# Optimization experiments

Hardware: AMD Instinct MI355X
Metric: run time of the kernel (lower is better)

Reference implementation:

```python
import jax, jax.numpy as jnp
import numpy as np

B = 1024           # number of jets (independent binary trees)
L = 10             # tree depth (levels); level j has B*2**j nodes
H = 128            # hidden size
FEAT = 7           # input features per node
LEVEL_SIZES = [B * 2**j for j in range(L)]
OFF = np.concatenate([[0], np.cumsum(LEVEL_SIZES)]).astype(int).tolist()
INNER = LEVEL_SIZES[:-1]                     # all non-bottom nodes are inner
COFF = np.concatenate([[0], np.cumsum(INNER)]).astype(int).tolist()


def _linear_init(key, fan_in, fan_out):
    return jax.random.normal(key, (fan_in, fan_out), jnp.float32) / np.sqrt(fan_in).astype(np.float32)


def setup_inputs() -> dict:
    key = jax.random.key(0)
    ks = jax.random.split(key, 6)
    contents = jax.random.normal(ks[0], (OFF[-1], FEAT), jnp.float32)
    # child indices are local to level j+1: node k at level j -> children (2k, 2k+1)
    ch = [np.stack([2 * np.arange(n), 2 * np.arange(n) + 1], axis=1) for n in INNER]
    children = jnp.asarray(np.concatenate(ch, axis=0), jnp.int32)
    return {
        "contents": contents,
        "children": children,
        "W_u": _linear_init(ks[1], FEAT, H), "b_u": jnp.zeros((H,), jnp.float32),
        "W_h": _linear_init(ks[2], 3 * H, H), "b_h": jnp.zeros((H,), jnp.float32),
        "W_z": _linear_init(ks[3], 4 * H, 4 * H), "b_z": jnp.zeros((4 * H,), jnp.float32),
        "W_r": _linear_init(ks[4], 3 * H, 3 * H), "b_r": jnp.zeros((3 * H,), jnp.float32),
        "conv_w": jnp.asarray([0.9], jnp.float32),
        "conv_b": jnp.asarray([0.01], jnp.float32),
    }


def reference(contents, children, W_u, b_u, W_h, b_h, W_z, b_z, W_r, b_r, conv_w, conv_b):
    def conv_chain(x):
        # relu(conv1x1(relu(conv1x1(relu(conv1x1(x)))))): Conv2d(1,1,1) == scalar scale + bias
        for _ in range(3):
            x = jax.nn.relu(conv_w[0] * x + conv_b[0])
        return x

    emb = None  # embeddings of the level below (level j+1)
    for j in reversed(range(L)):
        c = contents[OFF[j]:OFF[j + 1]]               # [N_j, FEAT]
        u = conv_chain(c @ W_u + b_u)                 # [N_j, H]
        if j == L - 1:                                # bottom level: all leaves
            emb = u
            continue
        ch = children[COFF[j]:COFF[j + 1]]            # [N_j, 2] indices into level j+1
        h_L = emb[ch[:, 0]]                           # gather left children
        h_R = emb[ch[:, 1]]                           # gather right children
        hhu = jnp.concatenate([h_L, h_R, u], axis=1)  # [N_j, 3H]
        r = jax.nn.sigmoid(hhu @ W_r + b_r)           # reset gate
        h_H = conv_chain((r * hhu) @ W_h + b_h)       # [N_j, H]
        z = jnp.concatenate([h_H, hhu], axis=1) @ W_z + b_z  # [N_j, 4H]
        g = jax.nn.softmax(
            jnp.stack([z[:, :H], z[:, H:2 * H], z[:, 2 * H:3 * H], z[:, 3 * H:]], axis=-1),
            axis=-1,
        )                                             # [N_j, H, 4] gate weights
        emb = g[..., 0] * h_H + g[..., 1] * h_L + g[..., 2] * h_R + g[..., 3] * u
    return emb.reshape(B, -1)                         # [B, H] root embeddings
```

## Files before the change

### kernel.cpp

```cpp
#include <hip/hip_runtime.h>
#include <hip/hip_bf16.h>

typedef _Float16 f16x8 __attribute__((ext_vector_type(8)));
typedef _Float16 f16x4 __attribute__((ext_vector_type(4)));
typedef float f32x4 __attribute__((ext_vector_type(4)));

#define H 128
#define FEAT 7
#define RB 64
#define NT 512

__device__ __forceinline__ float conv3(float x, float w, float b) {
    x = fmaxf(fmaf(w, x, b), 0.f);
    x = fmaxf(fmaf(w, x, b), 0.f);
    x = fmaxf(fmaf(w, x, b), 0.f);
    return x;
}
__device__ __forceinline__ float sigm(float x) {
    return __builtin_amdgcn_rcpf(1.f + __expf(-x));
}

__global__ __launch_bounds__(256) void pack_weights(
    const float* __restrict__ Wr, const float* __restrict__ Wh, const float* __restrict__ Wz,
    _Float16* __restrict__ Pr, _Float16* __restrict__ Ph, _Float16* __restrict__ Pz)
{
    int idx = blockIdx.x * 256 + threadIdx.x;
    if (idx < 384 * 384) {
        int k = idx / 384, n = idx % 384;
        Pr[((size_t)(k >> 3) * 384 + n) * 8 + (k & 7)] = (_Float16)Wr[idx];
    }
    if (idx < 384 * 128) {
        int k = idx / 128, n = idx % 128;
        Ph[((size_t)(k >> 3) * 128 + n) * 8 + (k & 7)] = (_Float16)Wh[idx];
    }
    if (idx < 512 * 512) {
        int k = idx / 512, n = idx % 512;
        Pz[((size_t)(k >> 3) * 512 + n) * 8 + (k & 7)] = (_Float16)Wz[idx];
    }
}

template<bool LEAF>
__global__ __launch_bounds__(NT, 2) void level_kernel(
    const float* __restrict__ contents,
    const int* __restrict__ children,
    const float* __restrict__ leafContents,
    const _Float16* __restrict__ embPrev,
    _Float16* __restrict__ embOut,
    float* __restrict__ finalOut,
    const float* __restrict__ Wu, const float* __restrict__ bu,
    const _Float16* __restrict__ Pr, const float* __restrict__ br,
    const _Float16* __restrict__ Ph, const float* __restrict__ bh,
    const _Float16* __restrict__ Pz, const float* __restrict__ bz,
    const float* __restrict__ convw, const float* __restrict__ convb)
{
    __shared__ __align__(16) _Float16 s_hhu[RB][392];
    __shared__ __align__(16) _Float16 s_x[RB][392];
    _Float16 (* const s_hH)[136] = (_Float16 (*)[136])&s_x[0][0];

    const int t = threadIdx.x;
    const int row0 = blockIdx.x * RB;
    const int col0 = t & 127;
    const int tq = t >> 7;
    const float cw = convw[0], cbv = convb[0];

    float wcol[FEAT];
#pragma unroll
    for (int k = 0; k < FEAT; k++) wcol[k] = Wu[k * H + col0];
    const float bucol = bu[col0];

#pragma unroll 4
    for (int i = 0; i < 16; i++) {
        int r = i * 4 + tq;
        const float* c = contents + (size_t)(row0 + r) * FEAT;
        float acc = bucol;
#pragma unroll
        for (int k = 0; k < FEAT; k++) acc = fmaf(c[k], wcol[k], acc);
        s_hhu[r][256 + col0] = (_Float16)conv3(acc, cw, cbv);
    }

    if (LEAF) {
#pragma unroll 4
        for (int i = 0; i < 32; i++) {
            int cr = i * 4 + tq;
            int child = children[row0 * 2 + cr];
            const float* c = leafContents + (size_t)child * FEAT;
            float acc = bucol;
#pragma unroll
            for (int k = 0; k < FEAT; k++) acc = fmaf(c[k], wcol[k], acc);
            s_hhu[cr >> 1][(cr & 1) * 128 + col0] = (_Float16)conv3(acc, cw, cbv);
        }
    } else {
        int rp = t >> 4, chunk = t & 15;
#pragma unroll
        for (int p = 0; p < 4; p++) {
            int cr = p * 32 + rp;
            int child = children[row0 * 2 + cr];
            uint4 v = *(const uint4*)(embPrev + (size_t)child * H + chunk * 8);
            *(uint4*)&s_hhu[cr >> 1][(cr & 1) * 128 + chunk * 8] = v;
        }
    }
    __syncthreads();

    const int lane = t & 63;
    const int w = t >> 6;
    const int q = lane >> 4;
    const int ln = lane & 15;

    {
        const f16x8* PB = (const f16x8*)Pr + (w * 48 + ln);
        f32x4 acc[3][4];
#pragma unroll
        for (int c = 0; c < 3; c++)
#pragma unroll
            for (int rt = 0; rt < 4; rt++) acc[c][rt] = (f32x4){0,0,0,0};
        f16x8 b[4];
#pragma unroll
        for (int rt = 0; rt < 4; rt++) b[rt] = *(const f16x8*)&s_hhu[rt * 16 + ln][q * 8];
        f16x8 an[3];
#pragma unroll
        for (int c = 0; c < 3; c++) an[c] = PB[(size_t)q * 384 + c * 16];
#pragma unroll
        for (int kk = 0; kk < 12; kk++) {
            f16x8 cb[4], ac[3];
#pragma unroll
            for (int rt = 0; rt < 4; rt++) cb[rt] = b[rt];
#pragma unroll
            for (int c = 0; c < 3; c++) ac[c] = an[c];
            if (kk < 11) {
                int kb = (kk + 1) * 4 + q;
#pragma unroll
                for (int c = 0; c < 3; c++) an[c] = PB[(size_t)kb * 384 + c * 16];
#pragma unroll
                for (int rt = 0; rt < 4; rt++)
                    b[rt] = *(const f16x8*)&s_hhu[rt * 16 + ln][(kk + 1) * 32 + q * 8];
            }
#pragma unroll
            for (int c = 0; c < 3; c++)
#pragma unroll
                for (int rt = 0; rt < 4; rt++)
                    acc[c][rt] = __builtin_amdgcn_mfma_f32_16x16x32_f16(ac[c], cb[rt], acc[c][rt], 0, 0, 0);
        }
#pragma unroll
        for (int c = 0; c < 3; c++) {
            int fb = w * 48 + c * 16 + q * 4;
            f32x4 bv = *(const f32x4*)&br[fb];
#pragma unroll
            for (int rt = 0; rt < 4; rt++) {
                int row = rt * 16 + ln;
                f16x4 hh = *(const f16x4*)&s_hhu[row][fb];
                f16x4 xv;
#pragma unroll
                for (int reg = 0; reg < 4; reg++) {
                    float rv = sigm(acc[c][rt][reg] + bv[reg]);
                    xv[reg] = (_Float16)(rv * (float)hh[reg]);
                }
                *(f16x4*)&s_x[row][fb] = xv;
            }
        }
    }
    __syncthreads();

    {
        const f16x8* PB = (const f16x8*)Ph + (w * 16 + ln);
        f32x4 acc[4];
#pragma unroll
        for (int rt = 0; rt < 4; rt++) acc[rt] = (f32x4){0,0,0,0};
        f16x8 b[4];
#pragma unroll
        for (int rt = 0; rt < 4; rt++) b[rt] = *(const f16x8*)&s_x[rt * 16 + ln][q * 8];
        f16x8 an = PB[(size_t)q * 128];
#pragma unroll
        for (int kk = 0; kk < 12; kk++) {
            f16x8 cb[4];
#pragma unroll
            for (int rt = 0; rt < 4; rt++) cb[rt] = b[rt];
            f16x8 ac = an;
            if (kk < 11) {
                int kb = (kk + 1) * 4 + q;
                an = PB[(size_t)kb * 128];
#pragma unroll
                for (int rt = 0; rt < 4; rt++)
                    b[rt] = *(const f16x8*)&s_x[rt * 16 + ln][(kk + 1) * 32 + q * 8];
            }
#pragma unroll
            for (int rt = 0; rt < 4; rt++)
                acc[rt] = __builtin_amdgcn_mfma_f32_16x16x32_f16(ac, cb[rt], acc[rt], 0, 0, 0);
        }
        float hv[4][4];
        int fb = w * 16 + q * 4;
        f32x4 bhv = *(const f32x4*)&bh[fb];
#pragma unroll
        for (int rt = 0; rt < 4; rt++)
#pragma unroll
            for (int reg = 0; reg < 4; reg++)
                hv[rt][reg] = conv3(acc[rt][reg] + bhv[reg], cw, cbv);
        __syncthreads();
#pragma unroll
        for (int rt = 0; rt < 4; rt++) {
            f16x4 hp;
#pragma unroll
            for (int reg = 0; reg < 4; reg++) hp[reg] = (_Float16)hv[rt][reg];
            *(f16x4*)&s_hH[rt * 16 + ln][fb] = hp;
        }
    }
    __syncthreads();

    {
        const int nb = w * 16;
        const f16x8* PL = (const f16x8*)Pz + nb + ln;
        f32x4 acc[4][4];
#pragma unroll
        for (int g = 0; g < 4; g++)
#pragma unroll
            for (int rt = 0; rt < 4; rt++) acc[g][rt] = (f32x4){0,0,0,0};
        f16x8 b[4];
#pragma unroll
        for (int rt = 0; rt < 4; rt++) b[rt] = *(const f16x8*)&s_hH[rt * 16 + ln][q * 8];
        f16x8 wn[4];
#pragma unroll
        for (int g = 0; g < 4; g++) wn[g] = PL[(size_t)q * 512 + g * 128];
#pragma unroll
        for (int kk = 0; kk < 16; kk++) {
            f16x8 cb[4], wc[4];
#pragma unroll
            for (int rt = 0; rt < 4; rt++) cb[rt] = b[rt];
#pragma unroll
            for (int g = 0; g < 4; g++) wc[g] = wn[g];
            if (kk < 15) {
                int kb = (kk + 1) * 4 + q;
#pragma unroll
                for (int g = 0; g < 4; g++) wn[g] = PL[(size_t)kb * 512 + g * 128];
                if (kk + 1 < 4) {
#pragma unroll
                    for (int rt = 0; rt < 4; rt++)
                        b[rt] = *(const f16x8*)&s_hH[rt * 16 + ln][(kk + 1) * 32 + q * 8];
                } else {
                    int k0 = (kk + 1) * 32 - 128;
#pragma unroll
                    for (int rt = 0; rt < 4; rt++)
                        b[rt] = *(const f16x8*)&s_hhu[rt * 16 + ln][k0 + q * 8];
                }
            }
#pragma unroll
            for (int g = 0; g < 4; g++)
#pragma unroll
                for (int rt = 0; rt < 4; rt++)
                    acc[g][rt] = __builtin_amdgcn_mfma_f32_16x16x32_f16(wc[g], cb[rt], acc[g][rt], 0, 0, 0);
        }
        int colb = nb + q * 4;
        f32x4 bz0 = *(const f32x4*)&bz[colb];
        f32x4 bz1 = *(const f32x4*)&bz[128 + colb];
        f32x4 bz2 = *(const f32x4*)&bz[256 + colb];
        f32x4 bz3 = *(const f32x4*)&bz[384 + colb];
#pragma unroll
        for (int rt = 0; rt < 4; rt++) {
            int row = rt * 16 + ln;
            f16x4 hH4 = *(const f16x4*)&s_hH[row][colb];
            f16x4 hL4 = *(const f16x4*)&s_hhu[row][colb];
            f16x4 hR4 = *(const f16x4*)&s_hhu[row][128 + colb];
            f16x4 u4  = *(const f16x4*)&s_hhu[row][256 + colb];
            size_t gidx = (size_t)(row0 + row) * H + colb;
            if (finalOut) {
                f32x4 ov;
#pragma unroll
                for (int reg = 0; reg < 4; reg++) {
                    float z0 = acc[0][rt][reg] + bz0[reg];
                    float z1 = acc[1][rt][reg] + bz1[reg];
                    float z2 = acc[2][rt][reg] + bz2[reg];
                    float z3 = acc[3][rt][reg] + bz3[reg];
                    float m = fmaxf(fmaxf(z0, z1), fmaxf(z2, z3));
                    float e0 = __expf(z0 - m), e1 = __expf(z1 - m), e2 = __expf(z2 - m), e3 = __expf(z3 - m);
                    float inv = __builtin_amdgcn_rcpf(e0 + e1 + e2 + e3);
                    ov[reg] = (e0 * (float)hH4[reg] + e1 * (float)hL4[reg] +
                               e2 * (float)hR4[reg] + e3 * (float)u4[reg]) * inv;
                }
                *(f32x4*)&finalOut[gidx] = ov;
            } else {
                f16x4 ev;
#pragma unroll
                for (int reg = 0; reg < 4; reg++) {
                    float z0 = acc[0][rt][reg] + bz0[reg];
                    float z1 = acc[1][rt][reg] + bz1[reg];
                    float z2 = acc[2][rt][reg] + bz2[reg];
                    float z3 = acc[3][rt][reg] + bz3[reg];
                    float m = fmaxf(fmaxf(z0, z1), fmaxf(z2, z3));
                    float e0 = __expf(z0 - m), e1 = __expf(z1 - m), e2 = __expf(z2 - m), e3 = __expf(z3 - m);
                    float inv = __builtin_amdgcn_rcpf(e0 + e1 + e2 + e3);
                    ev[reg] = (_Float16)((e0 * (float)hH4[reg] + e1 * (float)hL4[reg] +
                                          e2 * (float)hR4[reg] + e3 * (float)u4[reg]) * inv);
                }
                *(f16x4*)&embOut[gidx] = ev;
            }
        }
    }
}

extern "C" void kernel_launch(void* const* d_in, const int* in_sizes, int n_in,
                              void* d_out, int out_size, void* d_ws, size_t ws_size,
                              hipStream_t stream) {
    const float* contents = (const float*)d_in[0];
    const int*   children = (const int*)d_in[1];
    const float* Wu = (const float*)d_in[2];
    const float* bu = (const float*)d_in[3];
    const float* Wh = (const float*)d_in[4];
    const float* bh = (const float*)d_in[5];
    const float* Wz = (const float*)d_in[6];
    const float* bz = (const float*)d_in[7];
    const float* Wr = (const float*)d_in[8];
    const float* br = (const float*)d_in[9];
    const float* convw = (const float*)d_in[10];
    const float* convb = (const float*)d_in[11];
    float* out = (float*)d_out;

    _Float16* Pr = (_Float16*)d_ws;
    _Float16* Ph = Pr + 384 * 384;
    _Float16* Pz = Ph + 384 * 128;
    _Float16* bufA = (_Float16*)((char*)d_ws + (1 << 20));
    _Float16* bufB = bufA + (size_t)262144 * H;

    auto OFFS = [](int j) -> long long { return 1024LL * ((1LL << j) - 1); };

    pack_weights<<<(512 * 512 + 255) / 256, 256, 0, stream>>>(Wr, Wh, Wz, Pr, Ph, Pz);

    {
        int n = 1024 << 8;
        level_kernel<true><<<n / RB, NT, 0, stream>>>(
            contents + OFFS(8) * FEAT, children + OFFS(8) * 2,
            contents + OFFS(9) * FEAT, nullptr, bufA, nullptr,
            Wu, bu, Pr, br, Ph, bh, Pz, bz, convw, convb);
    }

    _Float16* prev = bufA;
    _Float16* cur  = bufB;
    for (int j = 7; j >= 0; j--) {
        int n = 1024 << j;
        level_kernel<false><<<n / RB, NT, 0, stream>>>(
            contents + OFFS(j) * FEAT, children + OFFS(j) * 2,
            nullptr, prev, cur, (j == 0 ? out : nullptr),
            Wu, bu, Pr, br, Ph, bh, Pz, bz, convw, convb);
        _Float16* tmp = prev; prev = cur; cur = tmp;
    }
}
```

Baseline: 834.2 us.

## Triple-buffer weight fragment prefetch two k-steps ahead and across GEMM stages

Weight fragments for the three MFMA GEMMs are now loaded two k-steps ahead into a three-slot register ring instead of one step ahead. The first two k-steps of each GEMM's weights are issued during the previous stage, before the embedding load phase and the epilogues, so global-load latency overlaps other work. Row and child indices in the embedding loops are made wave-uniform with readfirstlane so contents loads can become scalar loads. The deeper ring raises register pressure, which could reduce occupancy or cause spills.

```diff
diff --git a/kernel.cpp b/kernel.cpp
--- a/kernel.cpp
+++ b/kernel.cpp
@@ -63,6 +63,18 @@
     const int tq = t >> 7;
     const float cw = convw[0], cbv = convb[0];
 
+    const int lane = t & 63;
+    const int w = t >> 6;
+    const int q = lane >> 4;
+    const int ln = lane & 15;
+
+    const f16x8* PBc = (const f16x8*)Pr + (w * 48 + ln);
+    f16x8 awc[3][3];
+#pragma unroll
+    for (int c = 0; c < 3; c++) awc[0][c] = PBc[(size_t)q * 384 + c * 16];
+#pragma unroll
+    for (int c = 0; c < 3; c++) awc[1][c] = PBc[(size_t)(4 + q) * 384 + c * 16];
+
     float wcol[FEAT];
 #pragma unroll
     for (int k = 0; k < FEAT; k++) wcol[k] = Wu[k * H + col0];
@@ -71,23 +83,25 @@
 #pragma unroll 4
     for (int i = 0; i < 16; i++) {
         int r = i * 4 + tq;
-        const float* c = contents + (size_t)(row0 + r) * FEAT;
+        int ru = __builtin_amdgcn_readfirstlane(r);
+        const float* c = contents + (size_t)(row0 + ru) * FEAT;
         float acc = bucol;
 #pragma unroll
         for (int k = 0; k < FEAT; k++) acc = fmaf(c[k], wcol[k], acc);
-        s_hhu[r][256 + col0] = (_Float16)conv3(acc, cw, cbv);
+        s_hhu[ru][256 + col0] = (_Float16)conv3(acc, cw, cbv);
     }
 
     if (LEAF) {
 #pragma unroll 4
         for (int i = 0; i < 32; i++) {
             int cr = i * 4 + tq;
-            int child = children[row0 * 2 + cr];
+            int cru = __builtin_amdgcn_readfirstlane(cr);
+            int child = __builtin_amdgcn_readfirstlane(children[row0 * 2 + cru]);
             const float* c = leafContents + (size_t)child * FEAT;
             float acc = bucol;
 #pragma unroll
             for (int k = 0; k < FEAT; k++) acc = fmaf(c[k], wcol[k], acc);
-            s_hhu[cr >> 1][(cr & 1) * 128 + col0] = (_Float16)conv3(acc, cw, cbv);
+            s_hhu[cru >> 1][(cru & 1) * 128 + col0] = (_Float16)conv3(acc, cw, cbv);
         }
     } else {
         int rp = t >> 4, chunk = t & 15;
@@ -101,13 +115,10 @@
     }
     __syncthreads();
 
-    const int lane = t & 63;
-    const int w = t >> 6;
-    const int q = lane >> 4;
-    const int ln = lane & 15;
+    const f16x8* PBd = (const f16x8*)Ph + (w * 16 + ln);
+    f16x8 awd[3];
 
     {
-        const f16x8* PB = (const f16x8*)Pr + (w * 48 + ln);
         f32x4 acc[3][4];
 #pragma unroll
         for (int c = 0; c < 3; c++)
@@ -116,20 +127,17 @@
         f16x8 b[4];
 #pragma unroll
         for (int rt = 0; rt < 4; rt++) b[rt] = *(const f16x8*)&s_hhu[rt * 16 + ln][q * 8];
-        f16x8 an[3];
-#pragma unroll
-        for (int c = 0; c < 3; c++) an[c] = PB[(size_t)q * 384 + c * 16];
 #pragma unroll
         for (int kk = 0; kk < 12; kk++) {
-            f16x8 cb[4], ac[3];
+            if (kk + 2 < 12) {
+                int kb = (kk + 2) * 4 + q;
+#pragma unroll
+                for (int c = 0; c < 3; c++) awc[(kk + 2) % 3][c] = PBc[(size_t)kb * 384 + c * 16];
+            }
+            f16x8 cb[4];
 #pragma unroll
             for (int rt = 0; rt < 4; rt++) cb[rt] = b[rt];
-#pragma unroll
-            for (int c = 0; c < 3; c++) ac[c] = an[c];
             if (kk < 11) {
-                int kb = (kk + 1) * 4 + q;
-#pragma unroll
-                for (int c = 0; c < 3; c++) an[c] = PB[(size_t)kb * 384 + c * 16];
 #pragma unroll
                 for (int rt = 0; rt < 4; rt++)
                     b[rt] = *(const f16x8*)&s_hhu[rt * 16 + ln][(kk + 1) * 32 + q * 8];
@@ -138,8 +146,10 @@
             for (int c = 0; c < 3; c++)
 #pragma unroll
                 for (int rt = 0; rt < 4; rt++)
-                    acc[c][rt] = __builtin_amdgcn_mfma_f32_16x16x32_f16(ac[c], cb[rt], acc[c][rt], 0, 0, 0);
-        }
+                    acc[c][rt] = __builtin_amdgcn_mfma_f32_16x16x32_f16(awc[kk % 3][c], cb[rt], acc[c][rt], 0, 0, 0);
+        }
+        awd[0] = PBd[(size_t)q * 128];
+        awd[1] = PBd[(size_t)(4 + q) * 128];
 #pragma unroll
         for (int c = 0; c < 3; c++) {
             int fb = w * 48 + c * 16 + q * 4;
@@ -160,32 +170,38 @@
     }
     __syncthreads();
 
+    const f16x8* PBe = (const f16x8*)Pz + (w * 16 + ln);
+    f16x8 awe[3][4];
+
     {
-        const f16x8* PB = (const f16x8*)Ph + (w * 16 + ln);
         f32x4 acc[4];
 #pragma unroll
         for (int rt = 0; rt < 4; rt++) acc[rt] = (f32x4){0,0,0,0};
         f16x8 b[4];
 #pragma unroll
         for (int rt = 0; rt < 4; rt++) b[rt] = *(const f16x8*)&s_x[rt * 16 + ln][q * 8];
-        f16x8 an = PB[(size_t)q * 128];
 #pragma unroll
         for (int kk = 0; kk < 12; kk++) {
+            if (kk + 2 < 12) {
+                int kb = (kk + 2) * 4 + q;
+                awd[(kk + 2) % 3] = PBd[(size_t)kb * 128];
+            }
             f16x8 cb[4];
 #pragma unroll
             for (int rt = 0; rt < 4; rt++) cb[rt] = b[rt];
-            f16x8 ac = an;
             if (kk < 11) {
-                int kb = (kk + 1) * 4 + q;
-                an = PB[(size_t)kb * 128];
 #pragma unroll
                 for (int rt = 0; rt < 4; rt++)
                     b[rt] = *(const f16x8*)&s_x[rt * 16 + ln][(kk + 1) * 32 + q * 8];
             }
 #pragma unroll
             for (int rt = 0; rt < 4; rt++)
-                acc[rt] = __builtin_amdgcn_mfma_f32_16x16x32_f16(ac, cb[rt], acc[rt], 0, 0, 0);
-        }
+                acc[rt] = __builtin_amdgcn_mfma_f32_16x16x32_f16(awd[kk % 3], cb[rt], acc[rt], 0, 0, 0);
+        }
+#pragma unroll
+        for (int g = 0; g < 4; g++) awe[0][g] = PBe[(size_t)q * 512 + g * 128];
+#pragma unroll
+        for (int g = 0; g < 4; g++) awe[1][g] = PBe[(size_t)(4 + q) * 512 + g * 128];
         float hv[4][4];
         int fb = w * 16 + q * 4;
         f32x4 bhv = *(const f32x4*)&bh[fb];
@@ -207,7 +223,6 @@
 
     {
         const int nb = w * 16;
-        const f16x8* PL = (const f16x8*)Pz + nb + ln;
         f32x4 acc[4][4];
 #pragma unroll
         for (int g = 0; g < 4; g++)
@@ -216,20 +231,17 @@
         f16x8 b[4];
 #pragma unroll
         for (int rt = 0; rt < 4; rt++) b[rt] = *(const f16x8*)&s_hH[rt * 16 + ln][q * 8];
-        f16x8 wn[4];
-#pragma unroll
-        for (int g = 0; g < 4; g++) wn[g] = PL[(size_t)q * 512 + g * 128];
 #pragma unroll
         for (int kk = 0; kk < 16; kk++) {
-            f16x8 cb[4], wc[4];
+            if (kk + 2 < 16) {
+                int kb = (kk + 2) * 4 + q;
+#pragma unroll
+                for (int g = 0; g < 4; g++) awe[(kk + 2) % 3][g] = PBe[(size_t)kb * 512 + g * 128];
+            }
+            f16x8 cb[4];
 #pragma unroll
             for (int rt = 0; rt < 4; rt++) cb[rt] = b[rt];
-#pragma unroll
-            for (int g = 0; g < 4; g++) wc[g] = wn[g];
             if (kk < 15) {
-                int kb = (kk + 1) * 4 + q;
-#pragma unroll
-                for (int g = 0; g < 4; g++) wn[g] = PL[(size_t)kb * 512 + g * 128];
                 if (kk + 1 < 4) {
 #pragma unroll
                     for (int rt = 0; rt < 4; rt++)
@@ -245,7 +257,7 @@
             for (int g = 0; g < 4; g++)
 #pragma unroll
                 for (int rt = 0; rt < 4; rt++)
-                    acc[g][rt] = __builtin_amdgcn_mfma_f32_16x16x32_f16(wc[g], cb[rt], acc[g][rt], 0, 0, 0);
+                    acc[g][rt] = __builtin_amdgcn_mfma_f32_16x16x32_f16(awe[kk % 3][g], cb[rt], acc[g][rt], 0, 0, 0);
         }
         int colb = nb + q * 4;
         f32x4 bz0 = *(const f32x4*)&bz[colb];
```

After: 938.4 us. 12.5% more time.
